# Optimization experiments

Hardware: AMD Instinct MI355X
Metric: run time of the kernel (lower is better)

## Reference

```python
import jax, jax.numpy as jnp
import numpy as np

EPS = 1e-8  # torch F.cosine_similarity denominator clamp


def setup_inputs() -> dict:
    key = jax.random.key(0)
    k1, k2, k3 = jax.random.split(key, 3)
    B, F, T = 64, 512, 600
    data_label = jax.random.randint(k1, (B, F, T), 0, 100, dtype=jnp.int64)
    feature_a = jax.random.normal(k2, (B, F, T), dtype=jnp.float32)
    feature_b = jax.random.normal(k3, (B, F, T), dtype=jnp.float32)
    return {"data_label": data_label, "feature_a": feature_a, "feature_b": feature_b}


def _merge(feat, seg, merge_size):
    # feat: [B, F, T] -> segment-sum over time -> [B, M, F]
    ft = jnp.moveaxis(feat, 2, 0)  # [T, B, F]
    merged = jax.ops.segment_sum(ft, seg, num_segments=merge_size)  # [M, B, F]
    return jnp.moveaxis(merged, 1, 0)  # [B, M, F]


def reference(data_label, feature_a, feature_b):
    B, F, T = feature_a.shape
    merge_size = (T - 1) // 3 + 1
    # Original: f_merge[(i_time-1)//3] += f[i_time]; Python floor-div gives -1
    # for t=0, i.e. timestep 0 lands in the LAST bucket (negative indexing).
    seg = jnp.floor_divide(jnp.arange(T) - 1, 3) % merge_size  # [T]

    fa = _merge(feature_a, seg, merge_size)  # [B, M, F]
    fb = _merge(feature_b, seg, merge_size)  # [B, M, F]

    # Pairwise cosine similarity: cos[b, i, j] = cos(fa[b,i], fb[b,j])
    num = jnp.einsum('bmf,bnf->bmn', fa, fb)
    na = jnp.linalg.norm(fa, axis=-1)  # [B, M]
    nb = jnp.linalg.norm(fb, axis=-1)  # [B, M]
    cos = num / jnp.maximum(na[:, :, None] * nb[:, None, :], EPS)  # [B, M, M]

    # criterion: cross-entropy with diagonal (matched-time) targets,
    # mean over M per batch element, summed over batch (loss += criterion(...)).
    logp = jax.nn.log_softmax(cos, axis=-1)  # [B, M, M]
    idx = jnp.arange(cos.shape[1])
    diag = logp[:, idx, idx]  # [B, M]
    loss = jnp.sum(-jnp.mean(diag, axis=-1))
    return loss
```

## Files before the change

kernel.cpp:

```cpp
#include <hip/hip_runtime.h>
#include <hip/hip_bf16.h>
#include <math.h>

#define B_ 64
#define F_ 512
#define T_ 600
#define M_ 200
#define NFRAG 13

typedef __attribute__((ext_vector_type(8))) short bf16x8_t;
typedef __attribute__((ext_vector_type(4))) float f32x4_t;

static __device__ __forceinline__ unsigned short f2bf(float v) {
    __hip_bfloat16 h = __float2bfloat16(v);
    return *reinterpret_cast<unsigned short*>(&h);
}
static __device__ __forceinline__ float bf2f(unsigned short u) {
    return __uint_as_float(((unsigned)u) << 16);
}
static __device__ __forceinline__ float ssq8(uint4 v) {
    const unsigned short* s = (const unsigned short*)&v;
    float a = 0.f;
    #pragma unroll
    for (int i = 0; i < 8; ++i) { float x = bf2f(s[i]); a = fmaf(x, x, a); }
    return a;
}

__global__ __launch_bounds__(320)
void merge_t_kernel(const float* __restrict__ a, const float* __restrict__ b,
                    unsigned short* __restrict__ fa, unsigned short* __restrict__ fb,
                    float* __restrict__ out) {
    if (blockIdx.x == 0 && blockIdx.y == 0 && threadIdx.x == 0) out[0] = 0.f;

    const float* src = (blockIdx.y == 0) ? a : b;
    unsigned short* dst = (blockIdx.y == 0) ? fa : fb;
    int blk = blockIdx.x;
    int bb  = blk >> 3;
    int f0  = (blk & 7) * 64;

    __shared__ unsigned short tile[64][210];

    int t = threadIdx.x;
    const float* rowbase = src + (size_t)(bb * F_ + f0) * T_;

    #pragma unroll 5
    for (int i = 0; i < 10; ++i) {
        int task = t + i * 320;
        int r = task / 50;
        int j = task - r * 50;
        const float4* rp = (const float4*)(rowbase + (size_t)r * T_);
        float4 q0 = rp[3 * j];
        float4 q1 = rp[3 * j + 1];
        float4 q2 = rp[3 * j + 2];
        float s0 = q0.y + q0.z + q0.w;
        float s1 = q1.x + q1.y + q1.z;
        float s2 = q1.w + q2.x + q2.y;
        float s3;
        if (j < 49) {
            float4 q3 = rp[3 * j + 3];
            s3 = q2.z + q2.w + q3.x;
        } else {
            s3 = ((const float*)rp)[0] + q2.z + q2.w;
        }
        ushort2 p01 = make_ushort2(f2bf(s0), f2bf(s1));
        ushort2 p23 = make_ushort2(f2bf(s2), f2bf(s3));
        *(ushort2*)&tile[r][4 * j]     = p01;
        *(ushort2*)&tile[r][4 * j + 2] = p23;
    }
    __syncthreads();

    int lane8 = t & 7;
    int grp   = t >> 3;
    #pragma unroll
    for (int it = 0; it < 5; ++it) {
        int m = grp + it * 40;
        union { unsigned short s[8]; uint4 q; } u;
        #pragma unroll
        for (int k = 0; k < 8; ++k) u.s[k] = tile[lane8 * 8 + k][m];
        *(uint4*)(dst + (size_t)(bb * M_ + m) * F_ + f0 + lane8 * 8) = u.q;
    }
}

__global__ __launch_bounds__(256)
void fused_loss_kernel(const unsigned short* __restrict__ fa,
                       const unsigned short* __restrict__ fb,
                       float* __restrict__ out) {
    __shared__ unsigned short As[64][88];
    __shared__ unsigned short Bs[208][88];
    __shared__ float na_sq[64];
    __shared__ float nb_sq[208];
    __shared__ float wloss[4];

    int bb = blockIdx.y;
    int m0 = blockIdx.x * 64;
    const unsigned short* A  = fa + (size_t)bb * M_ * F_;
    const unsigned short* Bp = fb + (size_t)bb * M_ * F_;

    int t    = threadIdx.x;
    int lane = t & 63;
    int wave = t >> 6;
    int g    = lane >> 4;
    int c    = lane & 15;

    if (t < 64)  na_sq[t] = 0.f;
    if (t < 208) nb_sq[t] = 0.f;
    __syncthreads();

    f32x4_t acc[NFRAG];
    #pragma unroll
    for (int f = 0; f < NFRAG; ++f) acc[f] = (f32x4_t)(0.f);

    float assq0 = 0.f, assq1 = 0.f;
    const uint4 z4 = make_uint4(0, 0, 0, 0);

    for (int k0 = 0; k0 < F_; k0 += 64) {
        {
            int ar0 = t >> 3, kq = t & 7;
            int gm0 = m0 + ar0;
            uint4 v0 = z4;
            if (gm0 < M_) v0 = *(const uint4*)(A + (size_t)gm0 * F_ + k0 + kq * 8);
            *(uint4*)&As[ar0][kq * 8] = v0;
            assq0 += ssq8(v0);
            int ar1 = ar0 + 32;
            int gm1 = m0 + ar1;
            uint4 v1 = z4;
            if (gm1 < M_) v1 = *(const uint4*)(A + (size_t)gm1 * F_ + k0 + kq * 8);
            *(uint4*)&As[ar1][kq * 8] = v1;
            assq1 += ssq8(v1);
        }
        #pragma unroll
        for (int i = 0; i < 7; ++i) {
            int idx = t + (i << 8);
            if (idx < 1664) {
                int br = idx >> 3, kq = idx & 7;
                uint4 v = z4;
                if (br < M_) v = *(const uint4*)(Bp + (size_t)br * F_ + k0 + kq * 8);
                *(uint4*)&Bs[br][kq * 8] = v;
                if (br < M_) atomicAdd(&nb_sq[br], ssq8(v));
            }
        }
        __syncthreads();
        #pragma unroll
        for (int kk = 0; kk < 2; ++kk) {
            int kc = kk * 32 + g * 8;
            bf16x8_t af = *(const bf16x8_t*)&As[wave * 16 + c][kc];
            #pragma unroll
            for (int f = 0; f < NFRAG; ++f) {
                bf16x8_t bfr = *(const bf16x8_t*)&Bs[f * 16 + c][kc];
                acc[f] = __builtin_amdgcn_mfma_f32_16x16x32_bf16(af, bfr, acc[f], 0, 0, 0);
            }
        }
        __syncthreads();
    }

    #pragma unroll
    for (int off = 1; off <= 4; off <<= 1) {
        assq0 += __shfl_xor(assq0, off, 64);
        assq1 += __shfl_xor(assq1, off, 64);
    }
    if ((t & 7) == 0) {
        na_sq[t >> 3]        = assq0;
        na_sq[32 + (t >> 3)] = assq1;
    }
    __syncthreads();

    int m0w = m0 + wave * 16;
    float na_r[4];
    #pragma unroll
    for (int r = 0; r < 4; ++r) na_r[r] = sqrtf(na_sq[wave * 16 + g * 4 + r]);

    float mx[4] = {-INFINITY, -INFINITY, -INFINITY, -INFINITY};
    float diag_cos[4] = {0.f, 0.f, 0.f, 0.f};
    int f_diag = m0w >> 4;

    #pragma unroll
    for (int f = 0; f < NFRAG; ++f) {
        float nbv = sqrtf(nb_sq[f * 16 + c]);
        int col = f * 16 + c;
        bool colok = (col < M_);
        #pragma unroll
        for (int r = 0; r < 4; ++r) {
            float denom = fmaxf(na_r[r] * nbv, 1e-8f);
            float cv = acc[f][r] / denom;
            int row = m0w + g * 4 + r;
            if (f == f_diag && row < M_ && c == g * 4 + r) diag_cos[r] = cv;
            cv = colok ? cv : -INFINITY;
            acc[f][r] = cv;
            mx[r] = fmaxf(mx[r], cv);
        }
    }
    #pragma unroll
    for (int off = 1; off <= 8; off <<= 1)
        #pragma unroll
        for (int r = 0; r < 4; ++r)
            mx[r] = fmaxf(mx[r], __shfl_xor(mx[r], off, 64));

    float sm[4] = {0.f, 0.f, 0.f, 0.f};
    #pragma unroll
    for (int f = 0; f < NFRAG; ++f)
        #pragma unroll
        for (int r = 0; r < 4; ++r)
            sm[r] += __expf(acc[f][r] - mx[r]);
    #pragma unroll
    for (int off = 1; off <= 8; off <<= 1)
        #pragma unroll
        for (int r = 0; r < 4; ++r)
            sm[r] += __shfl_xor(sm[r], off, 64);

    float loss = 0.f;
    #pragma unroll
    for (int r = 0; r < 4; ++r) {
        int row = m0w + g * 4 + r;
        if (row < M_ && c == g * 4 + r) {
            float lse = mx[r] + __logf(sm[r]);
            loss -= (diag_cos[r] - lse) * (1.0f / (float)M_);
        }
    }
    #pragma unroll
    for (int off = 1; off <= 32; off <<= 1)
        loss += __shfl_xor(loss, off, 64);
    if (lane == 0) wloss[wave] = loss;
    __syncthreads();
    if (t == 0) atomicAdd(out, wloss[0] + wloss[1] + wloss[2] + wloss[3]);
}

extern "C" void kernel_launch(void* const* d_in, const int* in_sizes, int n_in,
                              void* d_out, int out_size, void* d_ws, size_t ws_size,
                              hipStream_t stream) {
    const float* a_in = (const float*)d_in[1];
    const float* b_in = (const float*)d_in[2];

    const size_t merged_elems = (size_t)B_ * M_ * F_;
    unsigned short* fa = (unsigned short*)d_ws;
    unsigned short* fb = fa + merged_elems;
    float* out = (float*)d_out;

    merge_t_kernel<<<dim3(B_ * (F_ / 64), 2), 320, 0, stream>>>(a_in, b_in, fa, fb, out);
    fused_loss_kernel<<<dim3(4, B_), 256, 0, stream>>>(fa, fb, out);
}
```

Measured before the change: 249.2 us.

## Store merged features in F-major layout, add separate norm kernel

The merge kernel no longer transposes through shared memory. It writes the bf16 time-merged sums straight into a [B,F,M] layout with simple coalesced stores. A new norm kernel computes the row norms from that layout, and the GEMM kernel now reads precomputed norms instead of accumulating squared sums with LDS atomics. The GEMM loaders transpose on the fly by packing pairs of F rows into the K-major shared tiles. This removes the LDS transpose and the atomics but adds a third launch and an extra read pass over the merged data.

```diff
diff --git a/kernel.cpp b/kernel.cpp
--- a/kernel.cpp
+++ b/kernel.cpp
@@ -18,83 +18,88 @@
 static __device__ __forceinline__ float bf2f(unsigned short u) {
     return __uint_as_float(((unsigned)u) << 16);
 }
-static __device__ __forceinline__ float ssq8(uint4 v) {
-    const unsigned short* s = (const unsigned short*)&v;
-    float a = 0.f;
-    #pragma unroll
-    for (int i = 0; i < 8; ++i) { float x = bf2f(s[i]); a = fmaf(x, x, a); }
-    return a;
-}
-
-__global__ __launch_bounds__(320)
-void merge_t_kernel(const float* __restrict__ a, const float* __restrict__ b,
-                    unsigned short* __restrict__ fa, unsigned short* __restrict__ fb,
-                    float* __restrict__ out) {
+
+__global__ __launch_bounds__(256)
+void merge_kernel(const float* __restrict__ a, const float* __restrict__ b,
+                  unsigned short* __restrict__ fa, unsigned short* __restrict__ fb,
+                  float* __restrict__ out) {
     if (blockIdx.x == 0 && blockIdx.y == 0 && threadIdx.x == 0) out[0] = 0.f;
 
     const float* src = (blockIdx.y == 0) ? a : b;
     unsigned short* dst = (blockIdx.y == 0) ? fa : fb;
-    int blk = blockIdx.x;
-    int bb  = blk >> 3;
-    int f0  = (blk & 7) * 64;
-
-    __shared__ unsigned short tile[64][210];
-
     int t = threadIdx.x;
-    const float* rowbase = src + (size_t)(bb * F_ + f0) * T_;
-
-    #pragma unroll 5
-    for (int i = 0; i < 10; ++i) {
-        int task = t + i * 320;
-        int r = task / 50;
-        int j = task - r * 50;
-        const float4* rp = (const float4*)(rowbase + (size_t)r * T_);
+    int base = blockIdx.x * 1024;
+
+    #pragma unroll
+    for (int i = 0; i < 4; ++i) {
+        int task = base + i * 256 + t;
+        int row = task / 50;
+        int j   = task - row * 50;
+        const float4* rp = (const float4*)(src + (size_t)row * T_);
         float4 q0 = rp[3 * j];
         float4 q1 = rp[3 * j + 1];
         float4 q2 = rp[3 * j + 2];
+        float4 q3 = (j < 49) ? rp[3 * j + 3] : rp[0];
         float s0 = q0.y + q0.z + q0.w;
         float s1 = q1.x + q1.y + q1.z;
         float s2 = q1.w + q2.x + q2.y;
-        float s3;
-        if (j < 49) {
-            float4 q3 = rp[3 * j + 3];
-            s3 = q2.z + q2.w + q3.x;
-        } else {
-            s3 = ((const float*)rp)[0] + q2.z + q2.w;
-        }
-        ushort2 p01 = make_ushort2(f2bf(s0), f2bf(s1));
-        ushort2 p23 = make_ushort2(f2bf(s2), f2bf(s3));
-        *(ushort2*)&tile[r][4 * j]     = p01;
-        *(ushort2*)&tile[r][4 * j + 2] = p23;
-    }
-    __syncthreads();
-
-    int lane8 = t & 7;
-    int grp   = t >> 3;
-    #pragma unroll
-    for (int it = 0; it < 5; ++it) {
-        int m = grp + it * 40;
-        union { unsigned short s[8]; uint4 q; } u;
-        #pragma unroll
-        for (int k = 0; k < 8; ++k) u.s[k] = tile[lane8 * 8 + k][m];
-        *(uint4*)(dst + (size_t)(bb * M_ + m) * F_ + f0 + lane8 * 8) = u.q;
-    }
+        float s3 = (j < 49) ? (q2.z + q2.w + q3.x)
+                            : (q3.x + q2.z + q2.w);
+        ushort4 o;
+        o.x = f2bf(s0); o.y = f2bf(s1); o.z = f2bf(s2); o.w = f2bf(s3);
+        *(ushort4*)(dst + (size_t)row * M_ + 4 * j) = o;
+    }
+}
+
+__global__ __launch_bounds__(256)
+void norm_kernel(const unsigned short* __restrict__ fa, const unsigned short* __restrict__ fb,
+                 float* __restrict__ na, float* __restrict__ nb) {
+    const unsigned short* src = (blockIdx.y == 0) ? fa : fb;
+    float*                dst = (blockIdx.y == 0) ? na : nb;
+    int bb = blockIdx.x;
+    int t  = threadIdx.x;
+    __shared__ unsigned short lds[64][200];
+
+    const unsigned short* S = src + (size_t)bb * F_ * M_;
+    float acc = 0.f;
+    for (int f0 = 0; f0 < F_; f0 += 64) {
+        #pragma unroll
+        for (int i = 0; i < 7; ++i) {
+            int idx = t + i * 256;
+            if (idx < 1600) {
+                int r  = idx / 25;
+                int c4 = idx - r * 25;
+                *(uint4*)&lds[r][c4 * 8] =
+                    *(const uint4*)(S + (size_t)(f0 + r) * M_ + c4 * 8);
+            }
+        }
+        __syncthreads();
+        if (t < M_) {
+            #pragma unroll 16
+            for (int f = 0; f < 64; ++f) {
+                float x = bf2f(lds[f][t]);
+                acc = fmaf(x, x, acc);
+            }
+        }
+        __syncthreads();
+    }
+    if (t < M_) dst[bb * M_ + t] = sqrtf(acc);
 }
 
 __global__ __launch_bounds__(256)
 void fused_loss_kernel(const unsigned short* __restrict__ fa,
                        const unsigned short* __restrict__ fb,
+                       const float* __restrict__ na_g,
+                       const float* __restrict__ nb_g,
                        float* __restrict__ out) {
     __shared__ unsigned short As[64][88];
     __shared__ unsigned short Bs[208][88];
-    __shared__ float na_sq[64];
-    __shared__ float nb_sq[208];
     __shared__ float wloss[4];
 
     int bb = blockIdx.y;
     int m0 = blockIdx.x * 64;
-    const unsigned short* A  = fa + (size_t)bb * M_ * F_;
-    const unsigned short* Bp = fb + (size_t)bb * M_ * F_;
+    const unsigned short* A  = fa + (size_t)bb * F_ * M_;
+    const unsigned short* Bp = fb + (size_t)bb * F_ * M_;
 
     int t    = threadIdx.x;
     int lane = t & 63;
@@ -102,41 +107,45 @@
     int g    = lane >> 4;
     int c    = lane & 15;
 
-    if (t < 64)  na_sq[t] = 0.f;
-    if (t < 208) nb_sq[t] = 0.f;
-    __syncthreads();
-
     f32x4_t acc[NFRAG];
     #pragma unroll
     for (int f = 0; f < NFRAG; ++f) acc[f] = (f32x4_t)(0.f);
 
-    float assq0 = 0.f, assq1 = 0.f;
     const uint4 z4 = make_uint4(0, 0, 0, 0);
 
     for (int k0 = 0; k0 < F_; k0 += 64) {
         {
-            int ar0 = t >> 3, kq = t & 7;
-            int gm0 = m0 + ar0;
-            uint4 v0 = z4;
-            if (gm0 < M_) v0 = *(const uint4*)(A + (size_t)gm0 * F_ + k0 + kq * 8);
-            *(uint4*)&As[ar0][kq * 8] = v0;
-            assq0 += ssq8(v0);
-            int ar1 = ar0 + 32;
-            int gm1 = m0 + ar1;
-            uint4 v1 = z4;
-            if (gm1 < M_) v1 = *(const uint4*)(A + (size_t)gm1 * F_ + k0 + kq * 8);
-            *(uint4*)&As[ar1][kq * 8] = v1;
-            assq1 += ssq8(v1);
-        }
-        #pragma unroll
-        for (int i = 0; i < 7; ++i) {
-            int idx = t + (i << 8);
-            if (idx < 1664) {
-                int br = idx >> 3, kq = idx & 7;
-                uint4 v = z4;
-                if (br < M_) v = *(const uint4*)(Bp + (size_t)br * F_ + k0 + kq * 8);
-                *(uint4*)&Bs[br][kq * 8] = v;
-                if (br < M_) atomicAdd(&nb_sq[br], ssq8(v));
+            int flp = t & 31;
+            int mg  = t >> 5;
+            bool mok = (m0 + 8 * mg + 8 <= M_);
+            int f = k0 + 2 * flp;
+            uint4 a0 = mok ? *(const uint4*)(A + (size_t)f       * M_ + m0 + 8 * mg) : z4;
+            uint4 a1 = mok ? *(const uint4*)(A + (size_t)(f + 1) * M_ + m0 + 8 * mg) : z4;
+            const unsigned short* s0 = (const unsigned short*)&a0;
+            const unsigned short* s1 = (const unsigned short*)&a1;
+            #pragma unroll
+            for (int i = 0; i < 8; ++i) {
+                unsigned pk = (unsigned)s0[i] | ((unsigned)s1[i] << 16);
+                *(unsigned*)&As[8 * mg + i][2 * flp] = pk;
+            }
+        }
+        #pragma unroll
+        for (int it = 0; it < 4; ++it) {
+            int idx = t + it * 256;
+            if (idx < 832) {
+                int flp = idx & 31;
+                int ng  = idx >> 5;
+                bool nok = (ng < 25);
+                int f = k0 + 2 * flp;
+                uint4 b0 = nok ? *(const uint4*)(Bp + (size_t)f       * M_ + 8 * ng) : z4;
+                uint4 b1 = nok ? *(const uint4*)(Bp + (size_t)(f + 1) * M_ + 8 * ng) : z4;
+                const unsigned short* s0 = (const unsigned short*)&b0;
+                const unsigned short* s1 = (const unsigned short*)&b1;
+                #pragma unroll
+                for (int i = 0; i < 8; ++i) {
+                    unsigned pk = (unsigned)s0[i] | ((unsigned)s1[i] << 16);
+                    *(unsigned*)&Bs[8 * ng + i][2 * flp] = pk;
+                }
             }
         }
         __syncthreads();
@@ -153,21 +162,13 @@
         __syncthreads();
     }
 
-    #pragma unroll
-    for (int off = 1; off <= 4; off <<= 1) {
-        assq0 += __shfl_xor(assq0, off, 64);
-        assq1 += __shfl_xor(assq1, off, 64);
-    }
-    if ((t & 7) == 0) {
-        na_sq[t >> 3]        = assq0;
-        na_sq[32 + (t >> 3)] = assq1;
-    }
-    __syncthreads();
-
     int m0w = m0 + wave * 16;
     float na_r[4];
     #pragma unroll
-    for (int r = 0; r < 4; ++r) na_r[r] = sqrtf(na_sq[wave * 16 + g * 4 + r]);
+    for (int r = 0; r < 4; ++r) {
+        int row = m0w + g * 4 + r;
+        na_r[r] = (row < M_) ? na_g[bb * M_ + row] : 1.0f;
+    }
 
     float mx[4] = {-INFINITY, -INFINITY, -INFINITY, -INFINITY};
     float diag_cos[4] = {0.f, 0.f, 0.f, 0.f};
@@ -175,9 +176,9 @@
 
     #pragma unroll
     for (int f = 0; f < NFRAG; ++f) {
-        float nbv = sqrtf(nb_sq[f * 16 + c]);
         int col = f * 16 + c;
         bool colok = (col < M_);
+        float nbv = colok ? nb_g[bb * M_ + col] : 1.0f;
         #pragma unroll
         for (int r = 0; r < 4; ++r) {
             float denom = fmaxf(na_r[r] * nbv, 1e-8f);
@@ -230,11 +231,14 @@
     const float* a_in = (const float*)d_in[1];
     const float* b_in = (const float*)d_in[2];
 
-    const size_t merged_elems = (size_t)B_ * M_ * F_;
+    const size_t merged_elems = (size_t)B_ * F_ * M_;
     unsigned short* fa = (unsigned short*)d_ws;
     unsigned short* fb = fa + merged_elems;
+    float* na = (float*)(fb + merged_elems);
+    float* nb = na + B_ * M_;
     float* out = (float*)d_out;
 
-    merge_t_kernel<<<dim3(B_ * (F_ / 64), 2), 320, 0, stream>>>(a_in, b_in, fa, fb, out);
-    fused_loss_kernel<<<dim3(4, B_), 256, 0, stream>>>(fa, fb, out);
-}
+    merge_kernel<<<dim3(1600, 2), 256, 0, stream>>>(a_in, b_in, fa, fb, out);
+    norm_kernel<<<dim3(B_, 2), 256, 0, stream>>>(fa, fb, na, nb);
+    fused_loss_kernel<<<dim3(4, B_), 256, 0, stream>>>(fa, fb, na, nb, out);
+}
```

Measured after the change: 256.9 us. 1.03x slower.
